# Performance work log

Hardware: AMD Instinct MI355X
Metric: run time of the kernel (lower is better)

Reference implementation:

```python
import jax, jax.numpy as jnp
import numpy as np

B, N, C, H = 4, 2048, 1024, 16
HD = C // H            # head dim = 64
HALF = HD // 2         # complex pairs per head = 32
VR = 32.0              # virtual_resolution
THETA = 10.0           # rope_theta


def _init_freqs():
    # mirrors init_3d_freqs_unified + per-axis replication with small noise
    rng = np.random.default_rng(0)
    idx = np.arange(HALF, dtype=np.float32)
    base = 1.0 / THETA ** (2.0 * idx / HD)                 # [HALF]
    angles = rng.uniform(0, 2 * np.pi, size=(H, 1)).astype(np.float32)
    per_head = base[None, :] * np.cos(angles)              # [H, HALF]
    freqs = np.repeat(per_head[None], 3, axis=0)           # [3, H, HALF]
    freqs = freqs + rng.normal(0, 0.01, freqs.shape).astype(np.float32)
    return jnp.asarray(freqs.reshape(3, H * HALF), dtype=jnp.float32)


def setup_inputs() -> dict:
    key = jax.random.key(0)
    ks = jax.random.split(key, 7)
    x = jax.random.normal(ks[0], (B, N, C), dtype=jnp.float32)
    t_x = jax.random.uniform(ks[1], (N,), dtype=jnp.float32)
    t_y = jax.random.uniform(ks[2], (N,), dtype=jnp.float32)
    t_z = jax.random.uniform(ks[3], (N,), dtype=jnp.float32)
    w_qkv = jax.random.normal(ks[4], (3 * C, C), dtype=jnp.float32) * (C ** -0.5)
    w_proj = jax.random.normal(ks[5], (C, C), dtype=jnp.float32) * (C ** -0.5)
    b_proj = jnp.zeros((C,), dtype=jnp.float32)
    freqs = _init_freqs()
    return {"x": x, "t_x": t_x, "t_y": t_y, "t_z": t_z,
            "w_qkv": w_qkv, "w_proj": w_proj, "b_proj": b_proj, "freqs": freqs}


def _normalize(t):
    # normalize_point_coords_3d with 'virtual_resolution'
    return (t - t.min()) / (t.max() - t.min() + 1e-8) * VR


def reference(x, t_x, t_y, t_z, w_qkv, w_proj, b_proj, freqs):
    # QKV projection (no bias)
    qkv = (x @ w_qkv.T).reshape(B, N, 3, H, HD).transpose(2, 0, 3, 1, 4)  # [3,B,H,N,HD]
    q, k, v = qkv[0], qkv[1], qkv[2]

    # mixed 3D RoPE angles: outer(t_axis, freqs[axis]) summed over axes
    tx, ty, tz = _normalize(t_x), _normalize(t_y), _normalize(t_z)
    ang = (tx[:, None] * freqs[0] + ty[:, None] * freqs[1] + tz[:, None] * freqs[2])  # [N, H*HALF]
    ang = ang.reshape(N, H, HALF).transpose(1, 0, 2)       # [H, N, HALF]
    cos, sin = jnp.cos(ang), jnp.sin(ang)

    def rotate(t):
        # complex multiply (a+ib)*(cos+isin) on even/odd pairs of last dim
        tr = t.reshape(B, H, N, HALF, 2)
        a, b = tr[..., 0], tr[..., 1]
        ra = a * cos - b * sin
        rb = a * sin + b * cos
        return jnp.stack([ra, rb], axis=-1).reshape(B, H, N, HD)

    q = rotate(q)
    k = rotate(k)

    scale = HD ** -0.5
    attn = jax.nn.softmax(jnp.einsum('bhnd,bhmd->bhnm', q * scale, k), axis=-1)
    out = jnp.einsum('bhnm,bhmd->bhnd', attn, v).transpose(0, 2, 1, 3).reshape(B, N, C)
    return out @ w_proj.T + b_proj
```

## Files before the change

### kernel.cpp

```cpp
#include <hip/hip_runtime.h>
#include <math.h>

#define BB 4
#define NN 2048
#define CC 1024
#define HH 16
#define HD 64
#define HALF 32
#define MM (BB*NN)
#define K3 (3*CC)
#define NF (HH*HALF)
#define NT (NN/64)

typedef __attribute__((ext_vector_type(8))) short bf16x8;
typedef __attribute__((ext_vector_type(4))) float f32x4;
typedef __attribute__((ext_vector_type(16))) float f32x16;
typedef __attribute__((ext_vector_type(4))) unsigned short u16x4;
typedef __attribute__((ext_vector_type(8))) unsigned short u16x8;
typedef __attribute__((ext_vector_type(4))) unsigned int u32x4;

#if __has_builtin(__builtin_amdgcn_exp2f)
#define EXP2(x) __builtin_amdgcn_exp2f(x)
#else
#define EXP2(x) exp2f(x)
#endif
#define AS1 __attribute__((address_space(1)))
#define AS3 __attribute__((address_space(3)))

__device__ __forceinline__ unsigned short f2bf(float f) {
    unsigned int u = __float_as_uint(f);
    unsigned int r = (u + 0x7FFFu + ((u >> 16) & 1u)) >> 16;
    return (unsigned short)r;
}

__global__ __launch_bounds__(256) void tnorm_kernel(const float* t_x, const float* t_y,
                                                    const float* t_z, float* tnorm) {
    int a = blockIdx.x;
    const float* t = (a == 0) ? t_x : ((a == 1) ? t_y : t_z);
    __shared__ float smn[256], smx[256];
    float mn = 1e30f, mx = -1e30f;
    for (int i = threadIdx.x; i < NN; i += 256) {
        float v = t[i];
        mn = fminf(mn, v);
        mx = fmaxf(mx, v);
    }
    smn[threadIdx.x] = mn; smx[threadIdx.x] = mx;
    __syncthreads();
    for (int s = 128; s > 0; s >>= 1) {
        if (threadIdx.x < s) {
            smn[threadIdx.x] = fminf(smn[threadIdx.x], smn[threadIdx.x + s]);
            smx[threadIdx.x] = fmaxf(smx[threadIdx.x], smx[threadIdx.x + s]);
        }
        __syncthreads();
    }
    float lo = smn[0];
    float sc = 32.0f / (smx[0] - lo + 1e-8f);
    for (int i = threadIdx.x; i < NN; i += 256)
        tnorm[a * NN + i] = (t[i] - lo) * sc;
}

__global__ __launch_bounds__(512) void angle_kernel(const float* freqs, const float* tnorm,
                                                    float* csT) {
    int n = blockIdx.x;
    int hf = threadIdx.x;
    float ang = tnorm[n] * freqs[hf]
              + tnorm[NN + n] * freqs[NF + hf]
              + tnorm[2 * NN + n] * freqs[2 * NF + hf];
    float2 cs;
    cs.x = cosf(ang);
    cs.y = sinf(ang);
    *(float2*)(csT + 2 * ((size_t)n * NF + hf)) = cs;
}

#define XBLK (MM * CC / 2048)
#define WQBLK (K3 * CC / 2048)
#define WPBLK (CC * CC / 2048)
__global__ __launch_bounds__(256) void cvt_all_kernel(const float* __restrict__ x,
                                                      const float* __restrict__ wq,
                                                      const float* __restrict__ wp,
                                                      unsigned short* __restrict__ xb,
                                                      unsigned short* __restrict__ wqb,
                                                      unsigned short* __restrict__ wpb) {
    int bid = blockIdx.x;
    const float* src;
    unsigned short* dst;
    if (bid < XBLK) { src = x; dst = xb; }
    else if (bid < XBLK + WQBLK) { src = wq; dst = wqb; bid -= XBLK; }
    else { src = wp; dst = wpb; bid -= XBLK + WQBLK; }
    int i = (bid * 256 + threadIdx.x) * 8;
    float4 a = *(const float4*)(src + i);
    float4 b = *(const float4*)(src + i + 4);
    u16x8 o;
    o[0] = f2bf(a.x); o[1] = f2bf(a.y); o[2] = f2bf(a.z); o[3] = f2bf(a.w);
    o[4] = f2bf(b.x); o[5] = f2bf(b.y); o[6] = f2bf(b.z); o[7] = f2bf(b.w);
    *(u16x8*)(dst + i) = o;
}

__global__ __launch_bounds__(256) void qkv_gemm_kernel(const unsigned short* __restrict__ A,
                                                       const unsigned short* __restrict__ Bw,
                                                       const float* __restrict__ csT,
                                                       unsigned short* __restrict__ qb,
                                                       unsigned short* __restrict__ kb,
                                                       unsigned short* __restrict__ vbT) {
    __shared__ unsigned short Asl[128 * 64];
    __shared__ unsigned short Bsl[128 * 64];
    const int tid = threadIdx.x;
    const int wv = tid >> 6, l = tid & 63;
    const int wm = wv >> 1, wn = wv & 1;
    const int lg = l >> 4, l15 = l & 15;
    const int m0 = blockIdx.x * 128, n0 = blockIdx.y * 128;

    f32x4 acc[4][4];
#pragma unroll
    for (int i = 0; i < 4; i++)
#pragma unroll
        for (int j = 0; j < 4; j++) acc[i][j] = f32x4{0.f, 0.f, 0.f, 0.f};

    for (int kt = 0; kt < CC; kt += 64) {
        __syncthreads();
#pragma unroll
        for (int i = 0; i < 4; i++) {
            int c = (wv * 4 + i) * 64 + l;
            int r = c >> 3, kc = c & 7;
            int sc = kt + ((kc ^ (r & 7)) * 8);
            __builtin_amdgcn_global_load_lds(
                (AS1 void*)(A + (size_t)(m0 + r) * CC + sc),
                (AS3 void*)(&Asl[(wv * 4 + i) * 512]), 16, 0, 0);
            __builtin_amdgcn_global_load_lds(
                (AS1 void*)(Bw + (size_t)(n0 + r) * CC + sc),
                (AS3 void*)(&Bsl[(wv * 4 + i) * 512]), 16, 0, 0);
        }
        __syncthreads();
#pragma unroll
        for (int kc = 0; kc < 2; kc++) {
            bf16x8 af[4], bfr[4];
#pragma unroll
            for (int mi = 0; mi < 4; mi++) {
                int r = wm * 64 + mi * 16 + l15;
                af[mi] = *(const bf16x8*)(&Asl[r * 64 + (((kc * 4 + lg) ^ (r & 7)) * 8)]);
            }
#pragma unroll
            for (int nj = 0; nj < 4; nj++) {
                int r = wn * 64 + nj * 16 + l15;
                bfr[nj] = *(const bf16x8*)(&Bsl[r * 64 + (((kc * 4 + lg) ^ (r & 7)) * 8)]);
            }
#pragma unroll
            for (int mi = 0; mi < 4; mi++)
#pragma unroll
                for (int nj = 0; nj < 4; nj++)
                    acc[mi][nj] = __builtin_amdgcn_mfma_f32_16x16x32_bf16(af[mi], bfr[nj], acc[mi][nj], 0, 0, 0);
        }
    }
    const int b_ = m0 >> 11;
    const int nrow0 = (m0 & (NN - 1));
#pragma unroll
    for (int nj = 0; nj < 4; nj++) {
        int oc = n0 + wn * 64 + nj * 16 + l15;
        int s = oc >> 10;
        int rr = oc & 1023;
        int h = rr >> 6;
        int d = rr & 63;
        int f = d >> 1;
#pragma unroll
        for (int mi = 0; mi < 4; mi++) {
            f32x4 v = acc[mi][nj];
            if (s == 2) {
                u16x4 vv;
#pragma unroll
                for (int reg = 0; reg < 4; reg++) vv[reg] = f2bf(v[reg]);
                int nb = nrow0 + wm * 64 + mi * 16 + lg * 4;
                *(u16x4*)(vbT + ((size_t)((b_ * HH + h) * HD + d)) * NN + nb) = vv;
            } else {
#pragma unroll
                for (int reg = 0; reg < 4; reg++) {
                    int m = m0 + wm * 64 + mi * 16 + lg * 4 + reg;
                    int n = m & (NN - 1);
                    float val = v[reg];
                    float partner = __shfl_xor(val, 1);
                    size_t base = (((size_t)(b_ * HH + h)) * NN + n) * HD + d;
                    float2 cs2 = *(const float2*)(csT + 2 * ((size_t)n * NF + h * HALF + f));
                    float res = ((d & 1) == 0) ? (val * cs2.x - partner * cs2.y)
                                               : (val * cs2.x + partner * cs2.y);
                    if (s == 0) res *= 0.18033688011112043f;
                    (s == 0 ? qb : kb)[base] = f2bf(res);
                }
            }
        }
    }
}

template<int BUF>
__device__ __forceinline__ void attn_iter(
    unsigned short* LB, bool do_stage, int wv, int l31,
    const unsigned short*& kn0, const unsigned short*& kn1,
    const unsigned short*& vn0, const unsigned short*& vn1,
    const int (&so)[4], const bf16x8 (&qfA)[4], const bf16x8 (&qfB)[4],
    const f32x16& Z, const bf16x8& ones,
    f32x16& OA0, f32x16& OA1, f32x16& OB0, f32x16& OB1,
    f32x16& SsA, f32x16& SsB) {
    if (do_stage) {
        const int nb = (BUF ^ 1) * 4096;
        __builtin_amdgcn_global_load_lds((AS1 void*)kn0, (AS3 void*)(&LB[nb + (wv * 2 + 0) * 512]), 16, 0, 0);
        __builtin_amdgcn_global_load_lds((AS1 void*)kn1, (AS3 void*)(&LB[nb + (wv * 2 + 1) * 512]), 16, 0, 0);
        __builtin_amdgcn_global_load_lds((AS1 void*)vn0, (AS3 void*)(&LB[8192 + nb + (wv * 2 + 0) * 512]), 16, 0, 0);
        __builtin_amdgcn_global_load_lds((AS1 void*)vn1, (AS3 void*)(&LB[8192 + nb + (wv * 2 + 1) * 512]), 16, 0, 0);
        kn0 += 4096; kn1 += 4096; vn0 += 64; vn1 += 64;
    }
    f32x16 sA0, sA1, sB0, sB1;
    __builtin_amdgcn_s_setprio(1);
    {
        bf16x8 a0 = *(const bf16x8*)(LB + BUF * 4096 + l31 * 64 + so[0]);
        bf16x8 a1 = *(const bf16x8*)(LB + BUF * 4096 + (32 + l31) * 64 + so[0]);
        sA0 = __builtin_amdgcn_mfma_f32_32x32x16_bf16(a0, qfA[0], Z, 0, 0, 0);
        sA1 = __builtin_amdgcn_mfma_f32_32x32x16_bf16(a1, qfA[0], Z, 0, 0, 0);
        sB0 = __builtin_amdgcn_mfma_f32_32x32x16_bf16(a0, qfB[0], Z, 0, 0, 0);
        sB1 = __builtin_amdgcn_mfma_f32_32x32x16_bf16(a1, qfB[0], Z, 0, 0, 0);
    }
#pragma unroll
    for (int dc = 1; dc < 4; dc++) {
        bf16x8 a0 = *(const bf16x8*)(LB + BUF * 4096 + l31 * 64 + so[dc]);
        bf16x8 a1 = *(const bf16x8*)(LB + BUF * 4096 + (32 + l31) * 64 + so[dc]);
        sA0 = __builtin_amdgcn_mfma_f32_32x32x16_bf16(a0, qfA[dc], sA0, 0, 0, 0);
        sA1 = __builtin_amdgcn_mfma_f32_32x32x16_bf16(a1, qfA[dc], sA1, 0, 0, 0);
        sB0 = __builtin_amdgcn_mfma_f32_32x32x16_bf16(a0, qfB[dc], sB0, 0, 0, 0);
        sB1 = __builtin_amdgcn_mfma_f32_32x32x16_bf16(a1, qfB[dc], sB1, 0, 0, 0);
    }
    __builtin_amdgcn_s_setprio(0);
#pragma unroll
    for (int r = 0; r < 16; r++) {
        sA0[r] = EXP2(sA0[r]); sA1[r] = EXP2(sA1[r]);
        sB0[r] = EXP2(sB0[r]); sB1[r] = EXP2(sB1[r]);
    }
#pragma unroll
    for (int r = 0; r < 8; r++) {
        unsigned u0, u1, u2, u3;
        asm("v_cvt_pk_bf16_f32 %0, %1, %2" : "=v"(u0) : "v"(sA0[2 * r]), "v"(sA0[2 * r + 1]));
        asm("v_cvt_pk_bf16_f32 %0, %1, %2" : "=v"(u1) : "v"(sA1[2 * r]), "v"(sA1[2 * r + 1]));
        asm("v_cvt_pk_bf16_f32 %0, %1, %2" : "=v"(u2) : "v"(sB0[2 * r]), "v"(sB0[2 * r + 1]));
        asm("v_cvt_pk_bf16_f32 %0, %1, %2" : "=v"(u3) : "v"(sB1[2 * r]), "v"(sB1[2 * r + 1]));
        sA0[2 * r] = __uint_as_float(u0);
        sA1[2 * r] = __uint_as_float(u1);
        sB0[2 * r] = __uint_as_float(u2);
        sB1[2 * r] = __uint_as_float(u3);
    }
    __builtin_amdgcn_s_setprio(1);
#pragma unroll
    for (int kc = 0; kc < 4; kc++) {
        const int bs = (kc & 1) * 8;
        bf16x8 pfA, pfB;
        {
            float e0 = (kc < 2) ? sA0[bs + 0] : sA1[bs + 0];
            float e4 = (kc < 2) ? sA0[bs + 4] : sA1[bs + 4];
            float e2 = (kc < 2) ? sA0[bs + 2] : sA1[bs + 2];
            float e6 = (kc < 2) ? sA0[bs + 6] : sA1[bs + 6];
            auto uA = __builtin_amdgcn_permlane32_swap(__float_as_uint(e0), __float_as_uint(e4), false, false);
            auto uB = __builtin_amdgcn_permlane32_swap(__float_as_uint(e2), __float_as_uint(e6), false, false);
            u32x4 t; t.x = uA[0]; t.y = uB[0]; t.z = uA[1]; t.w = uB[1];
            pfA = __builtin_bit_cast(bf16x8, t);
        }
        {
            float e0 = (kc < 2) ? sB0[bs + 0] : sB1[bs + 0];
            float e4 = (kc < 2) ? sB0[bs + 4] : sB1[bs + 4];
            float e2 = (kc < 2) ? sB0[bs + 2] : sB1[bs + 2];
            float e6 = (kc < 2) ? sB0[bs + 6] : sB1[bs + 6];
            auto uA = __builtin_amdgcn_permlane32_swap(__float_as_uint(e0), __float_as_uint(e4), false, false);
            auto uB = __builtin_amdgcn_permlane32_swap(__float_as_uint(e2), __float_as_uint(e6), false, false);
            u32x4 t; t.x = uA[0]; t.y = uB[0]; t.z = uA[1]; t.w = uB[1];
            pfB = __builtin_bit_cast(bf16x8, t);
        }
        bf16x8 va  = *(const bf16x8*)(LB + 8192 + BUF * 4096 + l31 * 64 + so[kc]);
        bf16x8 vb2 = *(const bf16x8*)(LB + 8192 + BUF * 4096 + (32 + l31) * 64 + so[kc]);
        OA0 = __builtin_amdgcn_mfma_f32_32x32x16_bf16(va,  pfA, OA0, 0, 0, 0);
        OA1 = __builtin_amdgcn_mfma_f32_32x32x16_bf16(vb2, pfA, OA1, 0, 0, 0);
        OB0 = __builtin_amdgcn_mfma_f32_32x32x16_bf16(va,  pfB, OB0, 0, 0, 0);
        OB1 = __builtin_amdgcn_mfma_f32_32x32x16_bf16(vb2, pfB, OB1, 0, 0, 0);
        SsA = __builtin_amdgcn_mfma_f32_32x32x16_bf16(ones, pfA, SsA, 0, 0, 0);
        SsB = __builtin_amdgcn_mfma_f32_32x32x16_bf16(ones, pfB, SsB, 0, 0, 0);
    }
    __builtin_amdgcn_s_setprio(0);
    __syncthreads();
}

__global__ __launch_bounds__(256, 2) void attn_mfma_kernel(const unsigned short* __restrict__ qbp,
                                                           const unsigned short* __restrict__ kbp,
                                                           const unsigned short* __restrict__ vtp,
                                                           unsigned short* __restrict__ aout) {
    __shared__ unsigned short LB[4 * 4096];
    const int tid = threadIdx.x;
    const int wv = tid >> 6;
    const int l = tid & 63;
    const int l31 = l & 31, hi = l >> 5;

    const int wg = blockIdx.x;
    const int Lidx = (wg & 7) * 64 + (wg >> 3);
    const int bh = Lidx >> 3;
    const int q0 = (Lidx & 7) * 256;

    const unsigned short* qp = qbp + (size_t)bh * (NN * HD);
    const unsigned short* kp = kbp + (size_t)bh * (NN * HD);
    const unsigned short* vp = vtp + (size_t)bh * (NN * HD);

    const int r0 = (wv * 2 + 0) * 8 + (l >> 3);
    const int r1 = (wv * 2 + 1) * 8 + (l >> 3);
    const int c0 = ((l & 7) ^ (r0 & 7)) * 8;
    const int c1 = ((l & 7) ^ (r1 & 7)) * 8;
    const unsigned short* kn0 = kp + r0 * HD + c0;
    const unsigned short* kn1 = kp + r1 * HD + c1;
    const unsigned short* vn0 = vp + (size_t)r0 * NN + c0;
    const unsigned short* vn1 = vp + (size_t)r1 * NN + c1;

    __builtin_amdgcn_global_load_lds((AS1 void*)kn0, (AS3 void*)(&LB[(wv * 2 + 0) * 512]), 16, 0, 0);
    __builtin_amdgcn_global_load_lds((AS1 void*)kn1, (AS3 void*)(&LB[(wv * 2 + 1) * 512]), 16, 0, 0);
    __builtin_amdgcn_global_load_lds((AS1 void*)vn0, (AS3 void*)(&LB[8192 + (wv * 2 + 0) * 512]), 16, 0, 0);
    __builtin_amdgcn_global_load_lds((AS1 void*)vn1, (AS3 void*)(&LB[8192 + (wv * 2 + 1) * 512]), 16, 0, 0);
    kn0 += 4096; kn1 += 4096; vn0 += 64; vn1 += 64;

    const unsigned short* qr = qp + (size_t)(q0 + wv * 64 + l31) * HD;
    bf16x8 qfA[4], qfB[4];
#pragma unroll
    for (int dc = 0; dc < 4; dc++) {
        qfA[dc] = *(const bf16x8*)(qr + dc * 16 + hi * 8);
        qfB[dc] = *(const bf16x8*)(qr + 32 * HD + dc * 16 + hi * 8);
    }

    int so[4];
#pragma unroll
    for (int i = 0; i < 4; i++) so[i] = ((2 * i + hi) ^ (l31 & 7)) * 8;

    f32x16 Z;
#pragma unroll
    for (int r = 0; r < 16; r++) Z[r] = 0.0f;
    f32x16 OA0 = Z, OA1 = Z, OB0 = Z, OB1 = Z, SsA = Z, SsB = Z;
    bf16x8 ones;
#pragma unroll
    for (int j = 0; j < 8; j++) ones[j] = (short)0x3F80;

    __syncthreads();

    for (int ktb = 0; ktb < NT; ktb += 2) {
        attn_iter<0>(LB, true, wv, l31, kn0, kn1, vn0, vn1, so, qfA, qfB,
                     Z, ones, OA0, OA1, OB0, OB1, SsA, SsB);
        attn_iter<1>(LB, ktb + 2 < NT, wv, l31, kn0, kn1, vn0, vn1, so, qfA, qfB,
                     Z, ones, OA0, OA1, OB0, OB1, SsA, SsB);
    }

    const int b_ = bh >> 4, hh = bh & 15;
    const float invA = 1.0f / SsA[0], invB = 1.0f / SsB[0];
    const size_t mrowA = (size_t)(b_ * NN + q0 + wv * 64 + l31) * CC + hh * HD;
    const size_t mrowB = mrowA + (size_t)32 * CC;
#pragma unroll
    for (int rq = 0; rq < 4; rq++) {
        u16x4 a0, a1, b0, b1;
#pragma unroll
        for (int j = 0; j < 4; j++) {
            a0[j] = f2bf(OA0[rq * 4 + j] * invA);
            a1[j] = f2bf(OA1[rq * 4 + j] * invA);
            b0[j] = f2bf(OB0[rq * 4 + j] * invB);
            b1[j] = f2bf(OB1[rq * 4 + j] * invB);
        }
        *(u16x4*)(aout + mrowA + rq * 8 + hi * 4) = a0;
        *(u16x4*)(aout + mrowA + 32 + rq * 8 + hi * 4) = a1;
        *(u16x4*)(aout + mrowB + rq * 8 + hi * 4) = b0;
        *(u16x4*)(aout + mrowB + 32 + rq * 8 + hi * 4) = b1;
    }
}

__global__ __launch_bounds__(256) void proj_gemm_kernel(const unsigned short* __restrict__ A,
                                                        const unsigned short* __restrict__ Bw,
                                                        const float* __restrict__ bp,
                                                        float* __restrict__ out) {
    __shared__ unsigned short Asl[128 * 64];
    __shared__ unsigned short Bsl[128 * 64];
    const int tid = threadIdx.x;
    const int wv = tid >> 6, l = tid & 63;
    const int wm = wv >> 1, wn = wv & 1;
    const int lg = l >> 4, l15 = l & 15;
    const int m0 = blockIdx.x * 128, n0 = blockIdx.y * 128;

    f32x4 acc[4][4];
#pragma unroll
    for (int i = 0; i < 4; i++)
#pragma unroll
        for (int j = 0; j < 4; j++) acc[i][j] = f32x4{0.f, 0.f, 0.f, 0.f};

    for (int kt = 0; kt < CC; kt += 64) {
        __syncthreads();
#pragma unroll
        for (int i = 0; i < 4; i++) {
            int c = (wv * 4 + i) * 64 + l;
            int r = c >> 3, kc = c & 7;
            int sc = kt + ((kc ^ (r & 7)) * 8);
            __builtin_amdgcn_global_load_lds(
                (AS1 void*)(A + (size_t)(m0 + r) * CC + sc),
                (AS3 void*)(&Asl[(wv * 4 + i) * 512]), 16, 0, 0);
            __builtin_amdgcn_global_load_lds(
                (AS1 void*)(Bw + (size_t)(n0 + r) * CC + sc),
                (AS3 void*)(&Bsl[(wv * 4 + i) * 512]), 16, 0, 0);
        }
        __syncthreads();
#pragma unroll
        for (int kc = 0; kc < 2; kc++) {
            bf16x8 af[4], bfr[4];
#pragma unroll
            for (int mi = 0; mi < 4; mi++) {
                int r = wm * 64 + mi * 16 + l15;
                af[mi] = *(const bf16x8*)(&Asl[r * 64 + (((kc * 4 + lg) ^ (r & 7)) * 8)]);
            }
#pragma unroll
            for (int nj = 0; nj < 4; nj++) {
                int r = wn * 64 + nj * 16 + l15;
                bfr[nj] = *(const bf16x8*)(&Bsl[r * 64 + (((kc * 4 + lg) ^ (r & 7)) * 8)]);
            }
#pragma unroll
            for (int mi = 0; mi < 4; mi++)
#pragma unroll
                for (int nj = 0; nj < 4; nj++)
                    acc[mi][nj] = __builtin_amdgcn_mfma_f32_16x16x32_bf16(af[mi], bfr[nj], acc[mi][nj], 0, 0, 0);
        }
    }
    float bias[4];
#pragma unroll
    for (int nj = 0; nj < 4; nj++) bias[nj] = bp[n0 + wn * 64 + nj * 16 + l15];
#pragma unroll
    for (int mi = 0; mi < 4; mi++)
#pragma unroll
        for (int nj = 0; nj < 4; nj++) {
            int oc = n0 + wn * 64 + nj * 16 + l15;
#pragma unroll
            for (int reg = 0; reg < 4; reg++) {
                int m = m0 + wm * 64 + mi * 16 + lg * 4 + reg;
                out[(size_t)m * CC + oc] = acc[mi][nj][reg] + bias[nj];
            }
        }
}

extern "C" void kernel_launch(void* const* d_in, const int* in_sizes, int n_in,
                              void* d_out, int out_size, void* d_ws, size_t ws_size,
                              hipStream_t stream) {
    const float* x      = (const float*)d_in[0];
    const float* t_x    = (const float*)d_in[1];
    const float* t_y    = (const float*)d_in[2];
    const float* t_z    = (const float*)d_in[3];
    const float* w_qkv  = (const float*)d_in[4];
    const float* w_proj = (const float*)d_in[5];
    const float* b_proj = (const float*)d_in[6];
    const float* freqs  = (const float*)d_in[7];
    float* out = (float*)d_out;

    unsigned short* xb     = (unsigned short*)d_ws;
    unsigned short* wqkvb  = xb + (size_t)MM * CC;
    unsigned short* wprojb = wqkvb + (size_t)K3 * CC;
    unsigned short* qbuf   = wprojb + (size_t)CC * CC;
    unsigned short* kbuf   = qbuf + (size_t)BB * HH * NN * HD;
    unsigned short* vbT    = kbuf + (size_t)BB * HH * NN * HD;
    unsigned short* attnb  = vbT + (size_t)BB * HH * NN * HD;
    float* csT   = (float*)(attnb + (size_t)MM * CC);
    float* tnorm = csT + (size_t)2 * NN * NF;

    tnorm_kernel<<<3, 256, 0, stream>>>(t_x, t_y, t_z, tnorm);
    angle_kernel<<<NN, 512, 0, stream>>>(freqs, tnorm, csT);
    cvt_all_kernel<<<XBLK + WQBLK + WPBLK, 256, 0, stream>>>(x, w_qkv, w_proj,
                                                             xb, wqkvb, wprojb);
    qkv_gemm_kernel<<<dim3(MM / 128, K3 / 128), 256, 0, stream>>>(xb, wqkvb, csT,
                                                                  qbuf, kbuf, vbT);
    attn_mfma_kernel<<<512, 256, 0, stream>>>(qbuf, kbuf, vbT, attnb);
    proj_gemm_kernel<<<dim3(MM / 128, CC / 128), 256, 0, stream>>>(attnb, wprojb, b_proj, out);
}
```

Before: 206.9 us.

## Double-buffer LDS tiles in QKV GEMM to overlap global loads with MFMA

After: 199.9 us. 1.04x faster.

```diff
diff --git a/kernel.cpp b/kernel.cpp
--- a/kernel.cpp
+++ b/kernel.cpp
@@ -102,55 +102,86 @@
                                                        unsigned short* __restrict__ qb,
                                                        unsigned short* __restrict__ kb,
                                                        unsigned short* __restrict__ vbT) {
-    __shared__ unsigned short Asl[128 * 64];
-    __shared__ unsigned short Bsl[128 * 64];
+    __shared__ unsigned short Asl[2][128 * 64];
+    __shared__ unsigned short Bsl[2][128 * 64];
     const int tid = threadIdx.x;
     const int wv = tid >> 6, l = tid & 63;
     const int wm = wv >> 1, wn = wv & 1;
     const int lg = l >> 4, l15 = l & 15;
     const int m0 = blockIdx.x * 128, n0 = blockIdx.y * 128;
 
+    const unsigned short* asrc[4];
+    const unsigned short* bsrc[4];
+#pragma unroll
+    for (int i = 0; i < 4; i++) {
+        int c = (wv * 4 + i) * 64 + l;
+        int r = c >> 3, kc = c & 7;
+        int sc = (kc ^ (r & 7)) * 8;
+        asrc[i] = A + (size_t)(m0 + r) * CC + sc;
+        bsrc[i] = Bw + (size_t)(n0 + r) * CC + sc;
+    }
+
+#define QSTAGE(buf) do { \
+    _Pragma("unroll") \
+    for (int i = 0; i < 4; i++) { \
+        __builtin_amdgcn_global_load_lds((AS1 void*)asrc[i], (AS3 void*)(&Asl[buf][(wv * 4 + i) * 512]), 16, 0, 0); \
+        __builtin_amdgcn_global_load_lds((AS1 void*)bsrc[i], (AS3 void*)(&Bsl[buf][(wv * 4 + i) * 512]), 16, 0, 0); \
+        asrc[i] += 64; bsrc[i] += 64; \
+    } \
+} while (0)
+
+#define QCOMPUTE(buf) do { \
+    _Pragma("unroll") \
+    for (int kc = 0; kc < 2; kc++) { \
+        bf16x8 af[4], bfr[4]; \
+        _Pragma("unroll") \
+        for (int mi = 0; mi < 4; mi++) { \
+            int r = wm * 64 + mi * 16 + l15; \
+            af[mi] = *(const bf16x8*)(&Asl[buf][r * 64 + (((kc * 4 + lg) ^ (r & 7)) * 8)]); \
+        } \
+        _Pragma("unroll") \
+        for (int nj = 0; nj < 4; nj++) { \
+            int r = wn * 64 + nj * 16 + l15; \
+            bfr[nj] = *(const bf16x8*)(&Bsl[buf][r * 64 + (((kc * 4 + lg) ^ (r & 7)) * 8)]); \
+        } \
+        _Pragma("unroll") \
+        for (int mi = 0; mi < 4; mi++) \
+            _Pragma("unroll") \
+            for (int nj = 0; nj < 4; nj++) \
+                acc[mi][nj] = __builtin_amdgcn_mfma_f32_16x16x32_bf16(af[mi], bfr[nj], acc[mi][nj], 0, 0, 0); \
+    } \
+} while (0)
+
+#define QSYNC_PRE() do { \
+    asm volatile("s_waitcnt vmcnt(8)" ::: "memory"); \
+    __builtin_amdgcn_sched_barrier(0); \
+    __builtin_amdgcn_s_barrier(); \
+    __builtin_amdgcn_sched_barrier(0); \
+} while (0)
+
+#define QSYNC_POST() do { \
+    __builtin_amdgcn_sched_barrier(0); \
+    __builtin_amdgcn_s_barrier(); \
+} while (0)
+
     f32x4 acc[4][4];
 #pragma unroll
     for (int i = 0; i < 4; i++)
 #pragma unroll
         for (int j = 0; j < 4; j++) acc[i][j] = f32x4{0.f, 0.f, 0.f, 0.f};
 
-    for (int kt = 0; kt < CC; kt += 64) {
-        __syncthreads();
-#pragma unroll
-        for (int i = 0; i < 4; i++) {
-            int c = (wv * 4 + i) * 64 + l;
-            int r = c >> 3, kc = c & 7;
-            int sc = kt + ((kc ^ (r & 7)) * 8);
-            __builtin_amdgcn_global_load_lds(
-                (AS1 void*)(A + (size_t)(m0 + r) * CC + sc),
-                (AS3 void*)(&Asl[(wv * 4 + i) * 512]), 16, 0, 0);
-            __builtin_amdgcn_global_load_lds(
-                (AS1 void*)(Bw + (size_t)(n0 + r) * CC + sc),
-                (AS3 void*)(&Bsl[(wv * 4 + i) * 512]), 16, 0, 0);
-        }
-        __syncthreads();
-#pragma unroll
-        for (int kc = 0; kc < 2; kc++) {
-            bf16x8 af[4], bfr[4];
-#pragma unroll
-            for (int mi = 0; mi < 4; mi++) {
-                int r = wm * 64 + mi * 16 + l15;
-                af[mi] = *(const bf16x8*)(&Asl[r * 64 + (((kc * 4 + lg) ^ (r & 7)) * 8)]);
-            }
-#pragma unroll
-            for (int nj = 0; nj < 4; nj++) {
-                int r = wn * 64 + nj * 16 + l15;
-                bfr[nj] = *(const bf16x8*)(&Bsl[r * 64 + (((kc * 4 + lg) ^ (r & 7)) * 8)]);
-            }
-#pragma unroll
-            for (int mi = 0; mi < 4; mi++)
-#pragma unroll
-                for (int nj = 0; nj < 4; nj++)
-                    acc[mi][nj] = __builtin_amdgcn_mfma_f32_16x16x32_bf16(af[mi], bfr[nj], acc[mi][nj], 0, 0, 0);
-        }
-    }
+    QSTAGE(0);
+    for (int ktb = 0; ktb < 16; ktb += 2) {
+        QSTAGE(1);
+        QSYNC_PRE();
+        QCOMPUTE(0);
+        QSYNC_POST();
+        QSTAGE(0);
+        QSYNC_PRE();
+        QCOMPUTE(1);
+        QSYNC_POST();
+    }
+
     const int b_ = m0 >> 11;
     const int nrow0 = (m0 & (NN - 1));
 #pragma unroll
@@ -187,6 +218,10 @@
             }
         }
     }
+#undef QSTAGE
+#undef QCOMPUTE
+#undef QSYNC_PRE
+#undef QSYNC_POST
 }
 
 template<int BUF>
```
